# Performance work log

Hardware: AMD Instinct MI355X
Metric: run time of the kernel (lower is better)

The kernel has to match this reference:

```python
import jax, jax.numpy as jnp
import numpy as np

EMBED = 1024

def setup_inputs() -> dict:
    key = jax.random.key(0)
    kx, kq, kk, kv = jax.random.split(key, 4)
    x = jax.random.normal(kx, (4, 2048, EMBED), dtype=jnp.float32)
    s = 1.0 / np.sqrt(EMBED)
    Wq = jax.random.normal(kq, (EMBED, EMBED), dtype=jnp.float32) * s
    Wk = jax.random.normal(kk, (EMBED, EMBED), dtype=jnp.float32) * s
    Wv = jax.random.normal(kv, (EMBED, EMBED), dtype=jnp.float32) * s
    return {"x": x, "Wq": Wq, "Wk": Wk, "Wv": Wv}

def reference(x, Wq, Wk, Wv):
    # x: [b, s, e]; nn.Linear(y) = y @ W.T, weights stored [out, in]
    Q = jnp.einsum('bse,oe->bso', x, Wq)
    K = jnp.einsum('bse,oe->bso', x, Wk)
    V = jnp.einsum('bse,oe->bso', x, Wv)
    scale = 1.0 / jnp.sqrt(jnp.asarray(x.shape[-1], x.dtype))
    energy = jnp.einsum('bqe,bke->bqk', Q, K) * scale  # [b, s, s]
    attention = jax.nn.softmax(energy, axis=-1)
    out = jnp.einsum('bqk,bke->bqe', attention, V)
    return out
```

## Files before the change

kernel.cpp:

```cpp
#include <hip/hip_runtime.h>
#include <stdint.h>


typedef __attribute__((ext_vector_type(8))) short bf16x8;
typedef __attribute__((ext_vector_type(4))) float f32x4;

__device__ __forceinline__ float bf2f(uint16_t u) {
    return __uint_as_float(((uint32_t)u) << 16);
}
__device__ __forceinline__ uint16_t f2bf(float f) {
    uint32_t u = __float_as_uint(f);
    uint32_t r = u + 0x7FFFu + ((u >> 16) & 1u);
    return (uint16_t)(r >> 16);
}

__device__ __forceinline__ void gll16(const void* g, void* l) {
    __builtin_amdgcn_global_load_lds(
        (const __attribute__((address_space(1))) uint32_t*)g,
        (__attribute__((address_space(3))) uint32_t*)l,
        16, 0, 0);
}

__global__ __launch_bounds__(256) void cast_all(const float* __restrict__ x,
                                                const float* __restrict__ Wq,
                                                const float* __restrict__ Wk,
                                                const float* __restrict__ Wv,
                                                uint16_t* __restrict__ xb,
                                                uint16_t* __restrict__ wqkvb,
                                                int NX4, int NW4) {
    int i = blockIdx.x * 256 + threadIdx.x;
    const float* src;
    uint16_t* dst;
    int off;
    if (i < NX4) {
        src = x; dst = xb; off = i;
    } else {
        int j = i - NX4;
        if (j >= 3 * NW4) return;
        int which = j / NW4;
        off = j - which * NW4;
        src = (which == 0) ? Wq : (which == 1) ? Wk : Wv;
        dst = wqkvb + (size_t)which * NW4 * 4;
    }
    float4 v = ((const float4*)src)[off];
    ushort4 o;
    o.x = f2bf(v.x); o.y = f2bf(v.y); o.z = f2bf(v.z); o.w = f2bf(v.w);
    ((ushort4*)dst)[off] = o;
}

__global__ __launch_bounds__(256) void softmax_rows(uint16_t* __restrict__ P) {
    const int n = 2048;
    uint16_t* row = P + (size_t)blockIdx.x * n;
    int tid = threadIdx.x;
    int w = tid >> 6, ln = tid & 63;
    float v[8];
    float m = -3.4e38f;
    #pragma unroll
    for (int i = 0; i < 8; i++) { v[i] = bf2f(row[tid + 256 * i]); m = fmaxf(m, v[i]); }
    #pragma unroll
    for (int o = 32; o >= 1; o >>= 1) m = fmaxf(m, __shfl_down(m, o, 64));
    __shared__ float smax[4], ssum[4];
    if (ln == 0) smax[w] = m;
    __syncthreads();
    m = fmaxf(fmaxf(smax[0], smax[1]), fmaxf(smax[2], smax[3]));
    float s = 0.f;
    #pragma unroll
    for (int i = 0; i < 8; i++) { v[i] = __expf(v[i] - m); s += v[i]; }
    #pragma unroll
    for (int o = 32; o >= 1; o >>= 1) s += __shfl_down(s, o, 64);
    if (ln == 0) ssum[w] = s;
    __syncthreads();
    s = ssum[0] + ssum[1] + ssum[2] + ssum[3];
    float inv = 1.f / s;
    #pragma unroll
    for (int i = 0; i < 8; i++) row[tid + 256 * i] = f2bf(v[i] * inv);
}

#define BM 128
#define BN 128
#define BK 32

template <typename OutT>
__global__ __launch_bounds__(256) void gemm_nt(const uint16_t* __restrict__ A,
                                               const uint16_t* __restrict__ B,
                                               OutT* __restrict__ C,
                                               int gx, int gy,
                                               long lda, long ldb, long ldc,
                                               int K, float alpha,
                                               long sA, long sB, long sC,
                                               uint16_t* __restrict__ VtP,
                                               int vcol0) {
    const int total = gridDim.x;
    const int n     = blockIdx.x;
    const int per   = total >> 3;
    const int g     = (n & 7) * per + (n >> 3);
    const int pb    = gx * gy;
    const int bz    = g / pb;
    const int r     = g - bz * pb;
    const int stpr  = gx >> 3;
    const int st    = r >> 6;
    const int w     = r & 63;
    const int sty   = st / stpr;
    const int stx   = st - sty * stpr;
    const int bx    = (stx << 3) + (w & 7);
    const int by    = (sty << 3) + (w >> 3);

    A += (long)bz * sA;
    B += (long)bz * sB;
    C += (long)bz * sC;

    __shared__ uint16_t As[3][BM * BK];
    __shared__ uint16_t Bs[3][BM * BK];

    const int tid  = threadIdx.x;
    const int m0   = by * BM;
    const int n0   = bx * BN;
    const int wave = tid >> 6;
    const int lane = tid & 63;
    const int quad = lane >> 4;
    const int l16  = lane & 15;
    const int wr   = (wave >> 1) * 64;
    const int wc   = (wave & 1) * 64;

    const int sr = tid >> 2;
    const int sc = (tid & 3) * 8;
    const uint16_t* Ag = A + (long)(m0 + sr) * lda + sc;
    const uint16_t* Bg = B + (long)(n0 + sr) * ldb + sc;
    const long rsA = 64 * lda;
    const long rsB = 64 * ldb;
    const int so0 = sr * BK + sc;
    const int so1 = (sr + 64) * BK + sc;

    const int nk = K / BK;

    gll16(Ag,       &As[0][so0]);
    gll16(Ag + rsA, &As[0][so1]);
    gll16(Bg,       &Bs[0][so0]);
    gll16(Bg + rsB, &Bs[0][so1]);
    Ag += BK; Bg += BK;
    gll16(Ag,       &As[1][so0]);
    gll16(Ag + rsA, &As[1][so1]);
    gll16(Bg,       &Bs[1][so0]);
    gll16(Bg + rsB, &Bs[1][so1]);
    Ag += BK; Bg += BK;

    f32x4 acc[4][4] = {};
    int cur = 0, pf = 2;

    for (int k = 0; k < nk; ++k) {
        if (k < nk - 1) {
            asm volatile("s_waitcnt vmcnt(4)\n\ts_barrier" ::: "memory");
        } else {
            asm volatile("s_waitcnt vmcnt(0)\n\ts_barrier" ::: "memory");
        }

        if (k + 2 < nk) {
            gll16(Ag,       &As[pf][so0]);
            gll16(Ag + rsA, &As[pf][so1]);
            gll16(Bg,       &Bs[pf][so0]);
            gll16(Bg + rsB, &Bs[pf][so1]);
            Ag += BK; Bg += BK;
        }

        const uint16_t* Ac = As[cur];
        const uint16_t* Bc = Bs[cur];
        const int ko = quad * 8;
        bf16x8 af[4], bfr[4];
        #pragma unroll
        for (int i = 0; i < 4; i++)
            af[i] = *(const bf16x8*)(&Ac[(wr + i * 16 + l16) * BK + ko]);
        #pragma unroll
        for (int j = 0; j < 4; j++)
            bfr[j] = *(const bf16x8*)(&Bc[(wc + j * 16 + l16) * BK + ko]);
        #pragma unroll
        for (int i = 0; i < 4; i++)
            #pragma unroll
            for (int j = 0; j < 4; j++)
                acc[i][j] = __builtin_amdgcn_mfma_f32_16x16x32_bf16(af[i], bfr[j], acc[i][j], 0, 0, 0);

        cur = (cur == 2) ? 0 : cur + 1;
        pf  = (pf  == 2) ? 0 : pf + 1;
    }

    if (VtP && n0 >= vcol0) {
        #pragma unroll
        for (int i = 0; i < 4; i++) {
            const int row0 = m0 + wr + i * 16 + quad * 4;
            const int b    = row0 >> 11;
            const int s    = row0 & 2047;
            #pragma unroll
            for (int j = 0; j < 4; j++) {
                const int e = n0 + wc + j * 16 + l16 - vcol0;
                ushort4 o;
                o.x = f2bf(acc[i][j][0]);
                o.y = f2bf(acc[i][j][1]);
                o.z = f2bf(acc[i][j][2]);
                o.w = f2bf(acc[i][j][3]);
                *(ushort4*)(VtP + ((long)b * 1024 + e) * 2048 + s) = o;
            }
        }
    } else {
        #pragma unroll
        for (int i = 0; i < 4; i++) {
            #pragma unroll
            for (int j = 0; j < 4; j++) {
                #pragma unroll
                for (int r4 = 0; r4 < 4; r4++) {
                    int row = m0 + wr + i * 16 + quad * 4 + r4;
                    int col = n0 + wc + j * 16 + l16;
                    float val = acc[i][j][r4] * alpha;
                    if constexpr (sizeof(OutT) == 2)
                        C[(long)row * ldc + col] = f2bf(val);
                    else
                        C[(long)row * ldc + col] = val;
                }
            }
        }
    }
}

extern "C" void kernel_launch(void* const* d_in, const int* in_sizes, int n_in,
                              void* d_out, int out_size, void* d_ws, size_t ws_size,
                              hipStream_t stream) {
    const float* x  = (const float*)d_in[0];
    const float* Wq = (const float*)d_in[1];
    const float* Wk = (const float*)d_in[2];
    const float* Wv = (const float*)d_in[3];
    float* out = (float*)d_out;

    const int Bn = 4, S = 2048, E = 1024;
    const long MS = (long)Bn * S;
    const int  N3 = 3 * E;

    char* ws = (char*)d_ws;
    uint16_t* xb    = (uint16_t*)ws;  ws += (size_t)MS * E * 2;
    uint16_t* wqkvb = (uint16_t*)ws;  ws += (size_t)N3 * E * 2;
    uint16_t* QKb   = (uint16_t*)ws;  ws += (size_t)MS * 2048 * 2;
    uint16_t* Vt    = (uint16_t*)ws;  ws += (size_t)Bn * E * S * 2;
    uint16_t* Pb    = (uint16_t*)ws;  ws += (size_t)Bn * S * S * 2;

    dim3 blk(256);

    {
        int NX4 = (int)(MS * E / 4);
        int NW4 = E * E / 4;
        int tot = NX4 + 3 * NW4;
        cast_all<<<dim3((tot + 255) / 256), blk, 0, stream>>>(
            x, Wq, Wk, Wv, xb, wqkvb, NX4, NW4);
    }

    {
        int gx = N3 / BN, gy = (int)(MS / BM);
        gemm_nt<uint16_t><<<dim3(gx * gy), blk, 0, stream>>>(
            xb, wqkvb, QKb, gx, gy, E, E, 2048, E, 1.f, 0, 0, 0,
            Vt, 2048);
    }

    {
        int gx = S / BN, gy = S / BM;
        gemm_nt<uint16_t><<<dim3(gx * gy * Bn), blk, 0, stream>>>(
            QKb, QKb + 1024, Pb, gx, gy, 2048, 2048, S, E, 0.03125f,
            (long)S * 2048, (long)S * 2048, (long)S * S,
            nullptr, 0);
    }

    softmax_rows<<<dim3(Bn * S), blk, 0, stream>>>(Pb);

    {
        int gx = E / BN, gy = S / BM;
        gemm_nt<float><<<dim3(gx * gy * Bn), blk, 0, stream>>>(
            Pb, Vt, out, gx, gy, S, S, E, S, 1.f,
            (long)S * S, (long)E * S, (long)S * E,
            nullptr, 0);
    }
}
```

Baseline: 264.6 us.

## Add 128x256-tile GEMM kernel for QKV projection and QK^T

Adds a new GEMM kernel with 128x256 output tiles: each wave computes 64x128, there are 32 accumulators per wave, and it uses double-buffered LDS instead of triple buffering. The kernel is used for the fused QKV projection and the QK^T energy GEMM. The larger tile raises arithmetic intensity per LDS and global load, at the cost of more registers and therefore lower occupancy. The PV GEMM keeps the original 128x128 kernel, with its unused V-transpose path removed.

```diff
diff --git a/kernel.cpp b/kernel.cpp
--- a/kernel.cpp
+++ b/kernel.cpp
@@ -76,9 +76,141 @@
     for (int i = 0; i < 8; i++) row[tid + 256 * i] = f2bf(v[i] * inv);
 }
 
-#define BM 128
-#define BN 128
 #define BK 32
+
+template <typename OutT>
+__global__ __launch_bounds__(256) void gemm_big(const uint16_t* __restrict__ A,
+                                                const uint16_t* __restrict__ B,
+                                                OutT* __restrict__ C,
+                                                int gx, int gy,
+                                                long lda, long ldb, long ldc,
+                                                int K, float alpha,
+                                                long sA, long sB, long sC,
+                                                uint16_t* __restrict__ VtP,
+                                                int vcol0) {
+    const int total = gridDim.x;
+    const int nblk  = blockIdx.x;
+    const int per   = total >> 3;
+    const int g     = (nblk & 7) * per + (nblk >> 3);
+    const int pb    = gx * gy;
+    const int bz    = g / pb;
+    const int r     = g - bz * pb;
+    const int stpr  = gx >> 2;
+    const int st    = r >> 4;
+    const int w16i  = r & 15;
+    const int sty   = st / stpr;
+    const int stx   = st - sty * stpr;
+    const int bx    = (stx << 2) + (w16i & 3);
+    const int by    = (sty << 2) + (w16i >> 2);
+
+    A += (long)bz * sA;
+    B += (long)bz * sB;
+    C += (long)bz * sC;
+
+    __shared__ uint16_t As[2][128 * BK];
+    __shared__ uint16_t Bs[2][256 * BK];
+
+    const int tid  = threadIdx.x;
+    const int m0   = by * 128;
+    const int n0   = bx * 256;
+    const int wave = tid >> 6;
+    const int lane = tid & 63;
+    const int quad = lane >> 4;
+    const int l16  = lane & 15;
+    const int wr   = (wave >> 1) * 64;
+    const int wc   = (wave & 1) * 128;
+
+    const int lr = lane >> 2;
+    const int lc = (lane & 3) * 8;
+    const uint16_t* Ag0 = A + (long)(m0 + wave * 32 + lr) * lda + lc;
+    const uint16_t* Ag1 = Ag0 + 16 * lda;
+    const int aso0 = (wave * 32 + lr) * BK + lc;
+    const int aso1 = aso0 + 16 * BK;
+    const uint16_t* Bg0 = B + (long)(n0 + wave * 64 + lr) * ldb + lc;
+    const int bso = (wave * 64 + lr) * BK + lc;
+
+    const int nk = K / BK;
+
+    gll16(Ag0, &As[0][aso0]);
+    gll16(Ag1, &As[0][aso1]);
+    #pragma unroll
+    for (int s = 0; s < 4; s++)
+        gll16(Bg0 + (long)(16 * s) * ldb, &Bs[0][bso + 16 * s * BK]);
+
+    f32x4 acc[4][8] = {};
+
+    for (int k = 0; k < nk; ++k) {
+        const int cur = k & 1;
+        __syncthreads();
+
+        if (k + 1 < nk) {
+            const int nxt = cur ^ 1;
+            const long ko = (long)(k + 1) * BK;
+            gll16(Ag0 + ko, &As[nxt][aso0]);
+            gll16(Ag1 + ko, &As[nxt][aso1]);
+            #pragma unroll
+            for (int s = 0; s < 4; s++)
+                gll16(Bg0 + (long)(16 * s) * ldb + ko, &Bs[nxt][bso + 16 * s * BK]);
+        }
+
+        const uint16_t* Ac = As[cur];
+        const uint16_t* Bc = Bs[cur];
+        const int ko = quad * 8;
+        bf16x8 af[4];
+        #pragma unroll
+        for (int i = 0; i < 4; i++)
+            af[i] = *(const bf16x8*)(&Ac[(wr + i * 16 + l16) * BK + ko]);
+        #pragma unroll
+        for (int jh = 0; jh < 2; jh++) {
+            bf16x8 bfr[4];
+            #pragma unroll
+            for (int jj = 0; jj < 4; jj++)
+                bfr[jj] = *(const bf16x8*)(&Bc[(wc + (jh * 4 + jj) * 16 + l16) * BK + ko]);
+            #pragma unroll
+            for (int jj = 0; jj < 4; jj++)
+                #pragma unroll
+                for (int i = 0; i < 4; i++)
+                    acc[i][jh * 4 + jj] = __builtin_amdgcn_mfma_f32_16x16x32_bf16(
+                        af[i], bfr[jj], acc[i][jh * 4 + jj], 0, 0, 0);
+        }
+    }
+
+    if (VtP && n0 >= vcol0) {
+        #pragma unroll
+        for (int i = 0; i < 4; i++) {
+            const int row0 = m0 + wr + i * 16 + quad * 4;
+            const int b    = row0 >> 11;
+            const int s    = row0 & 2047;
+            #pragma unroll
+            for (int j = 0; j < 8; j++) {
+                const int e = n0 + wc + j * 16 + l16 - vcol0;
+                ushort4 o;
+                o.x = f2bf(acc[i][j][0]);
+                o.y = f2bf(acc[i][j][1]);
+                o.z = f2bf(acc[i][j][2]);
+                o.w = f2bf(acc[i][j][3]);
+                *(ushort4*)(VtP + ((long)b * 1024 + e) * 2048 + s) = o;
+            }
+        }
+    } else {
+        #pragma unroll
+        for (int i = 0; i < 4; i++) {
+            #pragma unroll
+            for (int j = 0; j < 8; j++) {
+                #pragma unroll
+                for (int r4 = 0; r4 < 4; r4++) {
+                    int row = m0 + wr + i * 16 + quad * 4 + r4;
+                    int col = n0 + wc + j * 16 + l16;
+                    float val = acc[i][j][r4] * alpha;
+                    if constexpr (sizeof(OutT) == 2)
+                        C[(long)row * ldc + col] = f2bf(val);
+                    else
+                        C[(long)row * ldc + col] = val;
+                }
+            }
+        }
+    }
+}
 
 template <typename OutT>
 __global__ __launch_bounds__(256) void gemm_nt(const uint16_t* __restrict__ A,
@@ -87,9 +219,7 @@
                                                int gx, int gy,
                                                long lda, long ldb, long ldc,
                                                int K, float alpha,
-                                               long sA, long sB, long sC,
-                                               uint16_t* __restrict__ VtP,
-                                               int vcol0) {
+                                               long sA, long sB, long sC) {
     const int total = gridDim.x;
     const int n     = blockIdx.x;
     const int per   = total >> 3;
@@ -109,12 +239,12 @@
     B += (long)bz * sB;
     C += (long)bz * sC;
 
-    __shared__ uint16_t As[3][BM * BK];
-    __shared__ uint16_t Bs[3][BM * BK];
+    __shared__ uint16_t As[3][128 * BK];
+    __shared__ uint16_t Bs[3][128 * BK];
 
     const int tid  = threadIdx.x;
-    const int m0   = by * BM;
-    const int n0   = bx * BN;
+    const int m0   = by * 128;
+    const int n0   = bx * 128;
     const int wave = tid >> 6;
     const int lane = tid & 63;
     const int quad = lane >> 4;
@@ -182,38 +312,19 @@
         pf  = (pf  == 2) ? 0 : pf + 1;
     }
 
-    if (VtP && n0 >= vcol0) {
-        #pragma unroll
-        for (int i = 0; i < 4; i++) {
-            const int row0 = m0 + wr + i * 16 + quad * 4;
-            const int b    = row0 >> 11;
-            const int s    = row0 & 2047;
-            #pragma unroll
-            for (int j = 0; j < 4; j++) {
-                const int e = n0 + wc + j * 16 + l16 - vcol0;
-                ushort4 o;
-                o.x = f2bf(acc[i][j][0]);
-                o.y = f2bf(acc[i][j][1]);
-                o.z = f2bf(acc[i][j][2]);
-                o.w = f2bf(acc[i][j][3]);
-                *(ushort4*)(VtP + ((long)b * 1024 + e) * 2048 + s) = o;
-            }
-        }
-    } else {
-        #pragma unroll
-        for (int i = 0; i < 4; i++) {
-            #pragma unroll
-            for (int j = 0; j < 4; j++) {
-                #pragma unroll
-                for (int r4 = 0; r4 < 4; r4++) {
-                    int row = m0 + wr + i * 16 + quad * 4 + r4;
-                    int col = n0 + wc + j * 16 + l16;
-                    float val = acc[i][j][r4] * alpha;
-                    if constexpr (sizeof(OutT) == 2)
-                        C[(long)row * ldc + col] = f2bf(val);
-                    else
-                        C[(long)row * ldc + col] = val;
-                }
+    #pragma unroll
+    for (int i = 0; i < 4; i++) {
+        #pragma unroll
+        for (int j = 0; j < 4; j++) {
+            #pragma unroll
+            for (int r4 = 0; r4 < 4; r4++) {
+                int row = m0 + wr + i * 16 + quad * 4 + r4;
+                int col = n0 + wc + j * 16 + l16;
+                float val = acc[i][j][r4] * alpha;
+                if constexpr (sizeof(OutT) == 2)
+                    C[(long)row * ldc + col] = f2bf(val);
+                else
+                    C[(long)row * ldc + col] = val;
             }
         }
     }
@@ -250,15 +361,15 @@
     }
 
     {
-        int gx = N3 / BN, gy = (int)(MS / BM);
-        gemm_nt<uint16_t><<<dim3(gx * gy), blk, 0, stream>>>(
+        int gx = N3 / 256, gy = (int)(MS / 128);
+        gemm_big<uint16_t><<<dim3(gx * gy), blk, 0, stream>>>(
             xb, wqkvb, QKb, gx, gy, E, E, 2048, E, 1.f, 0, 0, 0,
             Vt, 2048);
     }
 
     {
-        int gx = S / BN, gy = S / BM;
-        gemm_nt<uint16_t><<<dim3(gx * gy * Bn), blk, 0, stream>>>(
+        int gx = S / 256, gy = S / 128;
+        gemm_big<uint16_t><<<dim3(gx * gy * Bn), blk, 0, stream>>>(
             QKb, QKb + 1024, Pb, gx, gy, 2048, 2048, S, E, 0.03125f,
             (long)S * 2048, (long)S * 2048, (long)S * S,
             nullptr, 0);
@@ -267,10 +378,9 @@
     softmax_rows<<<dim3(Bn * S), blk, 0, stream>>>(Pb);
 
     {
-        int gx = E / BN, gy = S / BM;
+        int gx = E / 128, gy = S / 128;
         gemm_nt<float><<<dim3(gx * gy * Bn), blk, 0, stream>>>(
             Pb, Vt, out, gx, gy, S, S, E, S, 1.f,
-            (long)S * S, (long)E * S, (long)S * E,
-            nullptr, 0);
-    }
-}
+            (long)S * S, (long)E * S, (long)S * E);
+    }
+}
```

Result: slower. 326.8 us (+23.5%).

## Fuse softmax into QK^T and PV GEMM epilogues with atomic row sums

Applied to the files above, without the earlier changes.

Removes the separate softmax kernel. The QK^T GEMM epilogue now writes exp(score*scale) as bf16 and atomically adds per-row partial sums into a buffer that the cast kernel zeroes. The PV GEMM epilogue divides each output row by its sum. The max subtraction is dropped, which relies on scores staying small enough not to overflow exp. The GEMM also moves from a triple-buffered pipeline with a custom vmcnt wait and swizzled block order to double buffering with __syncthreads and a plain 3D grid, which may cost some load/compute overlap and L2 locality.

```diff
diff --git a/kernel.cpp b/kernel.cpp
--- a/kernel.cpp
+++ b/kernel.cpp
@@ -27,7 +27,8 @@
                                                 const float* __restrict__ Wv,
                                                 uint16_t* __restrict__ xb,
                                                 uint16_t* __restrict__ wqkvb,
-                                                int NX4, int NW4) {
+                                                float* __restrict__ rowsum,
+                                                int NX4, int NW4, int NZ4) {
     int i = blockIdx.x * 256 + threadIdx.x;
     const float* src;
     uint16_t* dst;
@@ -36,11 +37,19 @@
         src = x; dst = xb; off = i;
     } else {
         int j = i - NX4;
-        if (j >= 3 * NW4) return;
-        int which = j / NW4;
-        off = j - which * NW4;
-        src = (which == 0) ? Wq : (which == 1) ? Wk : Wv;
-        dst = wqkvb + (size_t)which * NW4 * 4;
+        if (j < 3 * NW4) {
+            int which = j / NW4;
+            off = j - which * NW4;
+            src = (which == 0) ? Wq : (which == 1) ? Wk : Wv;
+            dst = wqkvb + (size_t)which * NW4 * 4;
+        } else {
+            int z = j - 3 * NW4;
+            if (z < NZ4) {
+                float4 zz = {0.f, 0.f, 0.f, 0.f};
+                ((float4*)rowsum)[z] = zz;
+            }
+            return;
+        }
     }
     float4 v = ((const float4*)src)[off];
     ushort4 o;
@@ -48,73 +57,29 @@
     ((ushort4*)dst)[off] = o;
 }
 
-__global__ __launch_bounds__(256) void softmax_rows(uint16_t* __restrict__ P) {
-    const int n = 2048;
-    uint16_t* row = P + (size_t)blockIdx.x * n;
-    int tid = threadIdx.x;
-    int w = tid >> 6, ln = tid & 63;
-    float v[8];
-    float m = -3.4e38f;
-    #pragma unroll
-    for (int i = 0; i < 8; i++) { v[i] = bf2f(row[tid + 256 * i]); m = fmaxf(m, v[i]); }
-    #pragma unroll
-    for (int o = 32; o >= 1; o >>= 1) m = fmaxf(m, __shfl_down(m, o, 64));
-    __shared__ float smax[4], ssum[4];
-    if (ln == 0) smax[w] = m;
-    __syncthreads();
-    m = fmaxf(fmaxf(smax[0], smax[1]), fmaxf(smax[2], smax[3]));
-    float s = 0.f;
-    #pragma unroll
-    for (int i = 0; i < 8; i++) { v[i] = __expf(v[i] - m); s += v[i]; }
-    #pragma unroll
-    for (int o = 32; o >= 1; o >>= 1) s += __shfl_down(s, o, 64);
-    if (ln == 0) ssum[w] = s;
-    __syncthreads();
-    s = ssum[0] + ssum[1] + ssum[2] + ssum[3];
-    float inv = 1.f / s;
-    #pragma unroll
-    for (int i = 0; i < 8; i++) row[tid + 256 * i] = f2bf(v[i] * inv);
-}
-
-#define BM 128
-#define BN 128
 #define BK 32
 
-template <typename OutT>
-__global__ __launch_bounds__(256) void gemm_nt(const uint16_t* __restrict__ A,
-                                               const uint16_t* __restrict__ B,
-                                               OutT* __restrict__ C,
-                                               int gx, int gy,
-                                               long lda, long ldb, long ldc,
-                                               int K, float alpha,
-                                               long sA, long sB, long sC,
-                                               uint16_t* __restrict__ VtP,
-                                               int vcol0) {
-    const int total = gridDim.x;
-    const int n     = blockIdx.x;
-    const int per   = total >> 3;
-    const int g     = (n & 7) * per + (n >> 3);
-    const int pb    = gx * gy;
-    const int bz    = g / pb;
-    const int r     = g - bz * pb;
-    const int stpr  = gx >> 3;
-    const int st    = r >> 6;
-    const int w     = r & 63;
-    const int sty   = st / stpr;
-    const int stx   = st - sty * stpr;
-    const int bx    = (stx << 3) + (w & 7);
-    const int by    = (sty << 3) + (w >> 3);
-
+template <int MODE, typename OutT>
+__global__ __launch_bounds__(256) void gemm2(const uint16_t* __restrict__ A,
+                                             const uint16_t* __restrict__ B,
+                                             OutT* __restrict__ C,
+                                             long lda, long ldb, long ldc,
+                                             int K, float alpha,
+                                             long sA, long sB, long sC,
+                                             uint16_t* __restrict__ VtP,
+                                             int vcol0,
+                                             float* __restrict__ rsum) {
+    const int bz = blockIdx.z;
     A += (long)bz * sA;
     B += (long)bz * sB;
     C += (long)bz * sC;
 
-    __shared__ uint16_t As[3][BM * BK];
-    __shared__ uint16_t Bs[3][BM * BK];
+    __shared__ uint16_t As[2][128 * BK];
+    __shared__ uint16_t Bs[2][128 * BK];
 
     const int tid  = threadIdx.x;
-    const int m0   = by * BM;
-    const int n0   = bx * BN;
+    const int m0   = blockIdx.y * 128;
+    const int n0   = blockIdx.x * 128;
     const int wave = tid >> 6;
     const int lane = tid & 63;
     const int quad = lane >> 4;
@@ -138,81 +103,101 @@
     gll16(Bg,       &Bs[0][so0]);
     gll16(Bg + rsB, &Bs[0][so1]);
     Ag += BK; Bg += BK;
-    gll16(Ag,       &As[1][so0]);
-    gll16(Ag + rsA, &As[1][so1]);
-    gll16(Bg,       &Bs[1][so0]);
-    gll16(Bg + rsB, &Bs[1][so1]);
-    Ag += BK; Bg += BK;
 
     f32x4 acc[4][4] = {};
-    int cur = 0, pf = 2;
 
     for (int k = 0; k < nk; ++k) {
-        if (k < nk - 1) {
-            asm volatile("s_waitcnt vmcnt(4)\n\ts_barrier" ::: "memory");
-        } else {
-            asm volatile("s_waitcnt vmcnt(0)\n\ts_barrier" ::: "memory");
-        }
-
-        if (k + 2 < nk) {
-            gll16(Ag,       &As[pf][so0]);
-            gll16(Ag + rsA, &As[pf][so1]);
-            gll16(Bg,       &Bs[pf][so0]);
-            gll16(Bg + rsB, &Bs[pf][so1]);
+        const int cur = k & 1;
+        __syncthreads();
+
+        if (k + 1 < nk) {
+            const int nxt = cur ^ 1;
+            gll16(Ag,       &As[nxt][so0]);
+            gll16(Ag + rsA, &As[nxt][so1]);
+            gll16(Bg,       &Bs[nxt][so0]);
+            gll16(Bg + rsB, &Bs[nxt][so1]);
             Ag += BK; Bg += BK;
         }
 
-        const uint16_t* Ac = As[cur];
-        const uint16_t* Bc = Bs[cur];
         const int ko = quad * 8;
         bf16x8 af[4], bfr[4];
         #pragma unroll
         for (int i = 0; i < 4; i++)
-            af[i] = *(const bf16x8*)(&Ac[(wr + i * 16 + l16) * BK + ko]);
+            af[i] = *(const bf16x8*)(&As[cur][(wr + i * 16 + l16) * BK + ko]);
         #pragma unroll
         for (int j = 0; j < 4; j++)
-            bfr[j] = *(const bf16x8*)(&Bc[(wc + j * 16 + l16) * BK + ko]);
+            bfr[j] = *(const bf16x8*)(&Bs[cur][(wc + j * 16 + l16) * BK + ko]);
         #pragma unroll
         for (int i = 0; i < 4; i++)
             #pragma unroll
             for (int j = 0; j < 4; j++)
                 acc[i][j] = __builtin_amdgcn_mfma_f32_16x16x32_bf16(af[i], bfr[j], acc[i][j], 0, 0, 0);
-
-        cur = (cur == 2) ? 0 : cur + 1;
-        pf  = (pf  == 2) ? 0 : pf + 1;
-    }
-
-    if (VtP && n0 >= vcol0) {
+    }
+
+    if constexpr (MODE == 0) {
+        if (VtP && n0 >= vcol0) {
+            #pragma unroll
+            for (int i = 0; i < 4; i++) {
+                const int row0 = m0 + wr + i * 16 + quad * 4;
+                const int b    = row0 >> 11;
+                const int s    = row0 & 2047;
+                #pragma unroll
+                for (int j = 0; j < 4; j++) {
+                    const int e = n0 + wc + j * 16 + l16 - vcol0;
+                    ushort4 o;
+                    o.x = f2bf(acc[i][j][0]);
+                    o.y = f2bf(acc[i][j][1]);
+                    o.z = f2bf(acc[i][j][2]);
+                    o.w = f2bf(acc[i][j][3]);
+                    *(ushort4*)(VtP + ((long)b * 1024 + e) * 2048 + s) = o;
+                }
+            }
+        } else {
+            #pragma unroll
+            for (int i = 0; i < 4; i++)
+                #pragma unroll
+                for (int j = 0; j < 4; j++)
+                    #pragma unroll
+                    for (int r4 = 0; r4 < 4; r4++) {
+                        int row = m0 + wr + i * 16 + quad * 4 + r4;
+                        int col = n0 + wc + j * 16 + l16;
+                        C[(long)row * ldc + col] = f2bf(acc[i][j][r4]);
+                    }
+        }
+    } else if constexpr (MODE == 1) {
+        float* rs = rsum + (long)bz * 2048;
         #pragma unroll
         for (int i = 0; i < 4; i++) {
-            const int row0 = m0 + wr + i * 16 + quad * 4;
-            const int b    = row0 >> 11;
-            const int s    = row0 & 2047;
-            #pragma unroll
-            for (int j = 0; j < 4; j++) {
-                const int e = n0 + wc + j * 16 + l16 - vcol0;
-                ushort4 o;
-                o.x = f2bf(acc[i][j][0]);
-                o.y = f2bf(acc[i][j][1]);
-                o.z = f2bf(acc[i][j][2]);
-                o.w = f2bf(acc[i][j][3]);
-                *(ushort4*)(VtP + ((long)b * 1024 + e) * 2048 + s) = o;
+            #pragma unroll
+            for (int r4 = 0; r4 < 4; r4++) {
+                const int row = m0 + wr + i * 16 + quad * 4 + r4;
+                float part = 0.f;
+                #pragma unroll
+                for (int j = 0; j < 4; j++) {
+                    const int col = n0 + wc + j * 16 + l16;
+                    float p = __expf(acc[i][j][r4] * alpha);
+                    C[(long)row * ldc + col] = f2bf(p);
+                    part += p;
+                }
+                part += __shfl_xor(part, 1, 64);
+                part += __shfl_xor(part, 2, 64);
+                part += __shfl_xor(part, 4, 64);
+                part += __shfl_xor(part, 8, 64);
+                if (l16 == 0) atomicAdd(&rs[row], part);
             }
         }
     } else {
+        const float* rs = rsum + (long)bz * 2048;
         #pragma unroll
         for (int i = 0; i < 4; i++) {
             #pragma unroll
-            for (int j = 0; j < 4; j++) {
-                #pragma unroll
-                for (int r4 = 0; r4 < 4; r4++) {
-                    int row = m0 + wr + i * 16 + quad * 4 + r4;
-                    int col = n0 + wc + j * 16 + l16;
-                    float val = acc[i][j][r4] * alpha;
-                    if constexpr (sizeof(OutT) == 2)
-                        C[(long)row * ldc + col] = f2bf(val);
-                    else
-                        C[(long)row * ldc + col] = val;
+            for (int r4 = 0; r4 < 4; r4++) {
+                const int row = m0 + wr + i * 16 + quad * 4 + r4;
+                const float inv = 1.0f / rs[row];
+                #pragma unroll
+                for (int j = 0; j < 4; j++) {
+                    const int col = n0 + wc + j * 16 + l16;
+                    C[(long)row * ldc + col] = acc[i][j][r4] * inv;
                 }
             }
         }
@@ -233,44 +218,44 @@
     const int  N3 = 3 * E;
 
     char* ws = (char*)d_ws;
-    uint16_t* xb    = (uint16_t*)ws;  ws += (size_t)MS * E * 2;
-    uint16_t* wqkvb = (uint16_t*)ws;  ws += (size_t)N3 * E * 2;
-    uint16_t* QKb   = (uint16_t*)ws;  ws += (size_t)MS * 2048 * 2;
-    uint16_t* Vt    = (uint16_t*)ws;  ws += (size_t)Bn * E * S * 2;
-    uint16_t* Pb    = (uint16_t*)ws;  ws += (size_t)Bn * S * S * 2;
+    uint16_t* xb     = (uint16_t*)ws;  ws += (size_t)MS * E * 2;
+    uint16_t* wqkvb  = (uint16_t*)ws;  ws += (size_t)N3 * E * 2;
+    uint16_t* QKb    = (uint16_t*)ws;  ws += (size_t)MS * 2048 * 2;
+    uint16_t* Vt     = (uint16_t*)ws;  ws += (size_t)Bn * E * S * 2;
+    uint16_t* Pb     = (uint16_t*)ws;  ws += (size_t)Bn * S * S * 2;
+    float*    rowsum = (float*)ws;     ws += (size_t)MS * 4;
 
     dim3 blk(256);
 
     {
         int NX4 = (int)(MS * E / 4);
         int NW4 = E * E / 4;
-        int tot = NX4 + 3 * NW4;
+        int NZ4 = (int)(MS / 4);
+        int tot = NX4 + 3 * NW4 + NZ4;
         cast_all<<<dim3((tot + 255) / 256), blk, 0, stream>>>(
-            x, Wq, Wk, Wv, xb, wqkvb, NX4, NW4);
-    }
-
-    {
-        int gx = N3 / BN, gy = (int)(MS / BM);
-        gemm_nt<uint16_t><<<dim3(gx * gy), blk, 0, stream>>>(
-            xb, wqkvb, QKb, gx, gy, E, E, 2048, E, 1.f, 0, 0, 0,
-            Vt, 2048);
-    }
-
-    {
-        int gx = S / BN, gy = S / BM;
-        gemm_nt<uint16_t><<<dim3(gx * gy * Bn), blk, 0, stream>>>(
-            QKb, QKb + 1024, Pb, gx, gy, 2048, 2048, S, E, 0.03125f,
+            x, Wq, Wk, Wv, xb, wqkvb, rowsum, NX4, NW4, NZ4);
+    }
+
+    {
+        dim3 g(N3 / 128, (int)(MS / 128), 1);
+        gemm2<0, uint16_t><<<g, blk, 0, stream>>>(
+            xb, wqkvb, QKb, E, E, 2048, E, 1.f, 0, 0, 0,
+            Vt, 2048, nullptr);
+    }
+
+    {
+        dim3 g(S / 128, S / 128, Bn);
+        gemm2<1, uint16_t><<<g, blk, 0, stream>>>(
+            QKb, QKb + 1024, Pb, 2048, 2048, S, E, 0.03125f,
             (long)S * 2048, (long)S * 2048, (long)S * S,
-            nullptr, 0);
-    }
-
-    softmax_rows<<<dim3(Bn * S), blk, 0, stream>>>(Pb);
-
-    {
-        int gx = E / BN, gy = S / BM;
-        gemm_nt<float><<<dim3(gx * gy * Bn), blk, 0, stream>>>(
-            Pb, Vt, out, gx, gy, S, S, E, S, 1.f,
+            nullptr, 0, rowsum);
+    }
+
+    {
+        dim3 g(E / 128, S / 128, Bn);
+        gemm2<2, float><<<g, blk, 0, stream>>>(
+            Pb, Vt, out, S, S, E, S, 1.f,
             (long)S * S, (long)E * S, (long)S * E,
-            nullptr, 0);
-    }
-}
+            nullptr, 0, rowsum);
+    }
+}
```

Result: slower. 284.0 us (+7.3%).
